# Performance work log

Measured on AMD Instinct MI355X. Metric: run time of the kernel, lower is better.

## Reference

```python
import jax, jax.numpy as jnp
import numpy as np

NUM_HEADS = 16
MODEL_DIM = 1024
DEPTH = MODEL_DIM // NUM_HEADS
B, S = 4, 1024


def setup_inputs() -> dict:
    key = jax.random.key(0)
    ks = jax.random.split(key, 12)
    sc = 1.0 / np.sqrt(MODEL_DIM)
    q = jax.random.normal(ks[0], (B, S, MODEL_DIM), jnp.float32)
    k = jax.random.normal(ks[1], (B, S, MODEL_DIM), jnp.float32)
    v = jax.random.normal(ks[2], (B, S, MODEL_DIM), jnp.float32)
    # binary padding mask, 1 = masked position (added as mask * -1e9)
    mask = (jax.random.uniform(ks[3], (B, 1, 1, S)) < 0.1).astype(jnp.float32)
    Wq = jax.random.normal(ks[4], (MODEL_DIM, MODEL_DIM), jnp.float32) * sc
    bq = jnp.zeros((MODEL_DIM,), jnp.float32)
    Wk = jax.random.normal(ks[5], (MODEL_DIM, MODEL_DIM), jnp.float32) * sc
    bk = jnp.zeros((MODEL_DIM,), jnp.float32)
    Wv = jax.random.normal(ks[6], (MODEL_DIM, MODEL_DIM), jnp.float32) * sc
    bv = jnp.zeros((MODEL_DIM,), jnp.float32)
    Wo = jax.random.normal(ks[7], (MODEL_DIM, MODEL_DIM), jnp.float32) * sc
    bo = jnp.zeros((MODEL_DIM,), jnp.float32)
    return dict(q=q, k=k, v=v, mask=mask, Wq=Wq, bq=bq, Wk=Wk, bk=bk,
                Wv=Wv, bv=bv, Wo=Wo, bo=bo)


def _split_head(x):
    b, s, _ = x.shape
    return x.reshape(b, s, NUM_HEADS, DEPTH).transpose(0, 2, 1, 3)


def reference(q, k, v, mask, Wq, bq, Wk, bk, Wv, bv, Wo, bo):
    Q = _split_head(q @ Wq + bq)   # (B,H,S,depth)
    K = _split_head(k @ Wk + bk)
    V = _split_head(v @ Wv + bv)
    # NOTE: original divides by k_dim (depth), NOT sqrt(depth) -- keep faithful
    logits = jnp.einsum('bhqd,bhkd->bhqk', Q, K) / jnp.float32(DEPTH)
    logits = logits + mask * (-1e9)
    attn = jax.nn.softmax(logits, axis=-1)         # (B,H,Sq,Sk)
    ctx = jnp.einsum('bhqk,bhkd->bhqd', attn, V)   # (B,H,S,depth)
    ctx = ctx.transpose(0, 2, 1, 3).reshape(q.shape[0], -1, MODEL_DIM)
    out = ctx @ Wo + bo
    return out, attn
```

## Files before the change

kernel.cpp:

```cpp
#include <hip/hip_runtime.h>
#include <stdint.h>
#include <stddef.h>

#define DEV __device__ __forceinline__

typedef __bf16 bf16_t;
typedef bf16_t bf16x8 __attribute__((ext_vector_type(8)));
typedef float f32x4 __attribute__((ext_vector_type(4)));
typedef unsigned short us4 __attribute__((ext_vector_type(4)));
typedef unsigned short us8 __attribute__((ext_vector_type(8)));

DEV float bf2f(unsigned short u) {
    union { unsigned int i; float f; } w; w.i = ((unsigned int)u) << 16; return w.f;
}
DEV unsigned short f2bf(float f) {
    union { unsigned int i; float f; } w; w.f = f;
    unsigned int u = w.i;
    return (unsigned short)((u + 0x7fffu + ((u >> 16) & 1u)) >> 16);
}

DEV void gl_lds16(const void* g, void* l) {
    __builtin_amdgcn_global_load_lds((const __attribute__((address_space(1))) void*)g,
                                     (__attribute__((address_space(3))) void*)l,
                                     16, 0, 0);
}

__global__ void __launch_bounds__(256)
cvt3(const float* __restrict__ s0, const float* __restrict__ s1, const float* __restrict__ s2,
     unsigned short* __restrict__ d0, unsigned short* __restrict__ d1, unsigned short* __restrict__ d2) {
    const float* src    = (blockIdx.z == 0) ? s0 : (blockIdx.z == 1) ? s1 : s2;
    unsigned short* dst = (blockIdx.z == 0) ? d0 : (blockIdx.z == 1) ? d1 : d2;
    int idx = (blockIdx.x * 256 + threadIdx.x) * 4;
    f32x4 v = *(const f32x4*)&src[idx];
    us4 o;
#pragma unroll
    for (int i = 0; i < 4; i++) o[i] = f2bf(v[i]);
    *(us4*)&dst[idx] = o;
}

__global__ void __launch_bounds__(256)
transpose_w(const float* __restrict__ W0, const float* __restrict__ W1,
            const float* __restrict__ W2, const float* __restrict__ W3,
            unsigned short* __restrict__ T0, unsigned short* __restrict__ T1,
            unsigned short* __restrict__ T2, unsigned short* __restrict__ T3) {
    const float* W    = (blockIdx.z == 0) ? W0 : (blockIdx.z == 1) ? W1 : (blockIdx.z == 2) ? W2 : W3;
    unsigned short* T = (blockIdx.z == 0) ? T0 : (blockIdx.z == 1) ? T1 : (blockIdx.z == 2) ? T2 : T3;
    __shared__ float t[32][33];
    int tx = threadIdx.x, ty = threadIdx.y;
    int k0 = blockIdx.x * 32, n0 = blockIdx.y * 32;
#pragma unroll
    for (int r = 0; r < 4; r++)
        t[ty + r * 8][tx] = W[(size_t)(k0 + ty + r * 8) * 1024 + n0 + tx];
    __syncthreads();
#pragma unroll
    for (int r = 0; r < 4; r++)
        T[(size_t)(n0 + ty + r * 8) * 1024 + k0 + tx] = f2bf(t[tx][ty + r * 8]);
}

__global__ void __launch_bounds__(256)
qkv_gemm(const unsigned short* __restrict__ Aq, const unsigned short* __restrict__ Ak,
         const unsigned short* __restrict__ Av,
         const unsigned short* __restrict__ BtQ, const unsigned short* __restrict__ BtK,
         const unsigned short* __restrict__ BtV,
         const float* __restrict__ biq, const float* __restrict__ bik,
         const float* __restrict__ biv,
         unsigned short* __restrict__ Qw, unsigned short* __restrict__ Kw,
         unsigned short* __restrict__ Vtw) {
    const int K = 1024;
    const unsigned short* A  = (blockIdx.z == 0) ? Aq  : (blockIdx.z == 1) ? Ak  : Av;
    const unsigned short* Bt = (blockIdx.z == 0) ? BtQ : (blockIdx.z == 1) ? BtK : BtV;
    const float* bias        = (blockIdx.z == 0) ? biq : (blockIdx.z == 1) ? bik : biv;
    unsigned short* Cout     = (blockIdx.z == 0) ? Qw  : (blockIdx.z == 1) ? Kw  : Vtw;
    const bool vmode = (blockIdx.z == 2);

    __shared__ __align__(16) unsigned short As[128 * 32];
    __shared__ __align__(16) unsigned short Bs[128 * 32];
    int tid = threadIdx.x, lane = tid & 63, wid = tid >> 6;
    int mBase = blockIdx.x * 128, nBase = blockIdx.y * 128;
    int wm = (wid >> 1) * 64, wn = (wid & 1) * 64;
    int c0 = lane & 15, quad = lane >> 4;

    f32x4 acc[4][4] = {};

    for (int k0 = 0; k0 < K; k0 += 32) {
        __syncthreads();
#pragma unroll
        for (int i = 0; i < 2; i++) {
            int cb = wid * 64 + 256 * i;
            int cc = cb + lane;
            int row = cc >> 2, kc = cc & 3;
            gl_lds16(A  + (size_t)(mBase + row) * K + k0 + kc * 8, &As[cb * 8]);
            gl_lds16(Bt + (size_t)(nBase + row) * K + k0 + kc * 8, &Bs[cb * 8]);
        }
        __syncthreads();
        bf16x8 af[4], bfr[4];
#pragma unroll
        for (int t = 0; t < 4; t++) {
            af[t]  = *(const bf16x8*)&As[(wm + t * 16 + c0) * 32 + quad * 8];
            bfr[t] = *(const bf16x8*)&Bs[(wn + t * 16 + c0) * 32 + quad * 8];
        }
#pragma unroll
        for (int mt = 0; mt < 4; mt++)
#pragma unroll
            for (int nt = 0; nt < 4; nt++)
                acc[mt][nt] = __builtin_amdgcn_mfma_f32_16x16x32_bf16(af[mt], bfr[nt], acc[mt][nt], 0, 0, 0);
    }

#pragma unroll
    for (int mt = 0; mt < 4; mt++) {
#pragma unroll
        for (int nt = 0; nt < 4; nt++) {
            int n = nBase + wn + nt * 16 + c0;
            float bv = bias[n];
            if (vmode) {
                int m0 = mBase + wm + mt * 16 + quad * 4;
                int b = m0 >> 10, s = m0 & 1023, h = n >> 6, d = n & 63;
                us4 pk;
#pragma unroll
                for (int r = 0; r < 4; r++) pk[r] = f2bf(acc[mt][nt][r] + bv);
                *(us4*)&Cout[((size_t)((b * 16 + h) * 64 + d)) * 1024 + s] = pk;
            } else {
#pragma unroll
                for (int r = 0; r < 4; r++) {
                    int m = mBase + wm + mt * 16 + quad * 4 + r;
                    int b = m >> 10, s = m & 1023, h = n >> 6, d = n & 63;
                    Cout[((size_t)((b * 16 + h) * 1024 + s)) * 64 + d] = f2bf(acc[mt][nt][r] + bv);
                }
            }
        }
    }
}

__global__ void __launch_bounds__(256)
out_gemm(const unsigned short* __restrict__ A,
         const unsigned short* __restrict__ Bt,
         const float* __restrict__ bias,
         float* __restrict__ Cout) {
    const int K = 1024;
    __shared__ __align__(16) unsigned short As[128 * 32];
    __shared__ __align__(16) unsigned short Bs[128 * 32];
    int tid = threadIdx.x, lane = tid & 63, wid = tid >> 6;
    int mBase = blockIdx.x * 128, nBase = blockIdx.y * 128;
    int wm = (wid >> 1) * 64, wn = (wid & 1) * 64;
    int c0 = lane & 15, quad = lane >> 4;

    f32x4 acc[4][4] = {};

    for (int k0 = 0; k0 < K; k0 += 32) {
        __syncthreads();
#pragma unroll
        for (int i = 0; i < 2; i++) {
            int cb = wid * 64 + 256 * i;
            int cc = cb + lane;
            int row = cc >> 2, kc = cc & 3;
            gl_lds16(A  + (size_t)(mBase + row) * K + k0 + kc * 8, &As[cb * 8]);
            gl_lds16(Bt + (size_t)(nBase + row) * K + k0 + kc * 8, &Bs[cb * 8]);
        }
        __syncthreads();
        bf16x8 af[4], bfr[4];
#pragma unroll
        for (int t = 0; t < 4; t++) {
            af[t]  = *(const bf16x8*)&As[(wm + t * 16 + c0) * 32 + quad * 8];
            bfr[t] = *(const bf16x8*)&Bs[(wn + t * 16 + c0) * 32 + quad * 8];
        }
#pragma unroll
        for (int mt = 0; mt < 4; mt++)
#pragma unroll
            for (int nt = 0; nt < 4; nt++)
                acc[mt][nt] = __builtin_amdgcn_mfma_f32_16x16x32_bf16(af[mt], bfr[nt], acc[mt][nt], 0, 0, 0);
    }
#pragma unroll
    for (int mt = 0; mt < 4; mt++)
#pragma unroll
        for (int nt = 0; nt < 4; nt++) {
            int n = nBase + wn + nt * 16 + c0;
            float bv = bias[n];
#pragma unroll
            for (int r = 0; r < 4; r++) {
                int m = mBase + wm + mt * 16 + quad * 4 + r;
                Cout[(size_t)m * 1024 + n] = acc[mt][nt][r] + bv;
            }
        }
}

__global__ void __launch_bounds__(256, 3)
attn_pv(const unsigned short* __restrict__ Qws,
        const unsigned short* __restrict__ Kws,
        const unsigned short* __restrict__ Vtw,
        const float* __restrict__ maskp,
        float* __restrict__ attnOut,
        unsigned short* __restrict__ ctx) {
    __shared__ __align__(16) unsigned short ldsP[17408];
    __shared__ float redbuf[4][16];

    int tid = threadIdx.x, lane = tid & 63, wid = tid >> 6;
    int c0 = lane & 15, quad = lane >> 4;
    int bh = blockIdx.y, b = bh >> 4, h = bh & 15;
    int q0 = blockIdx.x * 16;

    bf16x8 aq0, aq1;
    {
        const unsigned short* qp = Qws + ((size_t)bh * 1024 + q0 + c0) * 64 + quad * 8;
        aq0 = *(const bf16x8*)qp;
        aq1 = *(const bf16x8*)(qp + 32);
    }

    f32x4 acc[16] = {};

    for (int ch = 0; ch < 4; ch++) {
        __syncthreads();
#pragma unroll
        for (int i = 0; i < 8; i++) {
            int cb = wid * 64 + 256 * i;
            int cc = cb + lane;
            int row = cc >> 3, kc = cc & 7;
            gl_lds16(Kws + ((size_t)bh * 1024 + ch * 256 + row) * 64 + kc * 8, &ldsP[cb * 8]);
        }
        __syncthreads();
#pragma unroll
        for (int nt = 0; nt < 4; nt++) {
            int srow = wid * 64 + nt * 16 + c0;
            const unsigned short* kp = &ldsP[srow * 64 + quad * 8];
            bf16x8 b0 = *(const bf16x8*)kp;
            bf16x8 b1 = *(const bf16x8*)(kp + 32);
            int ai = ch * 4 + nt;
            acc[ai] = __builtin_amdgcn_mfma_f32_16x16x32_bf16(aq0, b0, acc[ai], 0, 0, 0);
            acc[ai] = __builtin_amdgcn_mfma_f32_16x16x32_bf16(aq1, b1, acc[ai], 0, 0, 0);
        }
    }

    float lmax[4] = {-3e38f, -3e38f, -3e38f, -3e38f};
#pragma unroll
    for (int i = 0; i < 16; i++) {
        int col = (i >> 2) * 256 + wid * 64 + (i & 3) * 16 + c0;
        float mval = maskp[b * 1024 + col] * (-1e9f);
#pragma unroll
        for (int r = 0; r < 4; r++) {
            float v = acc[i][r] * (1.0f / 64.0f) + mval;
            acc[i][r] = v;
            lmax[r] = fmaxf(lmax[r], v);
        }
    }
#pragma unroll
    for (int st = 1; st < 16; st <<= 1) {
#pragma unroll
        for (int r = 0; r < 4; r++) lmax[r] = fmaxf(lmax[r], __shfl_xor(lmax[r], st, 64));
    }
    if (c0 == 0) {
#pragma unroll
        for (int r = 0; r < 4; r++) redbuf[wid][quad * 4 + r] = lmax[r];
    }
    __syncthreads();
    float rmax[4];
#pragma unroll
    for (int r = 0; r < 4; r++) {
        int row = quad * 4 + r;
        rmax[r] = fmaxf(fmaxf(redbuf[0][row], redbuf[1][row]), fmaxf(redbuf[2][row], redbuf[3][row]));
    }
    float lsum[4] = {0.f, 0.f, 0.f, 0.f};
#pragma unroll
    for (int i = 0; i < 16; i++) {
#pragma unroll
        for (int r = 0; r < 4; r++) {
            float e = __expf(acc[i][r] - rmax[r]);
            acc[i][r] = e;
            lsum[r] += e;
        }
    }
#pragma unroll
    for (int st = 1; st < 16; st <<= 1) {
#pragma unroll
        for (int r = 0; r < 4; r++) lsum[r] += __shfl_xor(lsum[r], st, 64);
    }
    __syncthreads();
    if (c0 == 0) {
#pragma unroll
        for (int r = 0; r < 4; r++) redbuf[wid][quad * 4 + r] = lsum[r];
    }
    __syncthreads();
    float rinv[4];
#pragma unroll
    for (int r = 0; r < 4; r++) {
        int row = quad * 4 + r;
        rinv[r] = 1.0f / (redbuf[0][row] + redbuf[1][row] + redbuf[2][row] + redbuf[3][row]);
    }

    size_t gbase = ((size_t)bh * 1024 + q0) * 1024;
#pragma unroll
    for (int i = 0; i < 16; i++) {
        int kk = (i >> 2) * 64 + (i & 3) * 16 + c0;
        int col = (i >> 2) * 256 + wid * 64 + (i & 3) * 16 + c0;
        int kks = kk ^ (quad << 3);
#pragma unroll
        for (int r = 0; r < 4; r++) {
            int row = quad * 4 + r;
            float pv = acc[i][r] * rinv[r];
            attnOut[gbase + (size_t)row * 1024 + col] = pv;
            ldsP[wid * 4352 + row * 272 + kks] = f2bf(pv);
        }
    }

    const unsigned short* vbase = Vtw + ((size_t)(bh * 64 + wid * 16 + c0)) * 1024 + quad * 8;
    bf16x8 vcur[8], vnxt[8];
#pragma unroll
    for (int j = 0; j < 8; j++)
        vcur[j] = *(const bf16x8*)&vbase[(j >> 1) * 64 + (j & 1) * 32];
    __syncthreads();

    f32x4 ctx0 = {}, ctx1 = {};
#pragma unroll
    for (int ch = 0; ch < 4; ch++) {
        if (ch < 3) {
#pragma unroll
            for (int j = 0; j < 8; j++)
                vnxt[j] = *(const bf16x8*)&vbase[(ch + 1) * 256 + (j >> 1) * 64 + (j & 1) * 32];
        }
#pragma unroll
        for (int wv = 0; wv < 4; wv++) {
            int kidx0 = (ch * 64 + quad * 8) ^ ((c0 >> 2) << 3);
            int kidx1 = (ch * 64 + 32 + quad * 8) ^ ((c0 >> 2) << 3);
            bf16x8 a0 = *(const bf16x8*)&ldsP[wv * 4352 + c0 * 272 + kidx0];
            bf16x8 a1 = *(const bf16x8*)&ldsP[wv * 4352 + c0 * 272 + kidx1];
            ctx0 = __builtin_amdgcn_mfma_f32_16x16x32_bf16(a0, vcur[wv * 2 + 0], ctx0, 0, 0, 0);
            ctx1 = __builtin_amdgcn_mfma_f32_16x16x32_bf16(a1, vcur[wv * 2 + 1], ctx1, 0, 0, 0);
        }
#pragma unroll
        for (int j = 0; j < 8; j++) vcur[j] = vnxt[j];
    }
    f32x4 ctxacc = ctx0 + ctx1;

#pragma unroll
    for (int r = 0; r < 4; r++) {
        int s = q0 + quad * 4 + r;
        ctx[((size_t)(b * 1024 + s)) * 1024 + h * 64 + wid * 16 + c0] = f2bf(ctxacc[r]);
    }
}

extern "C" void kernel_launch(void* const* d_in, const int* in_sizes, int n_in,
                              void* d_out, int out_size, void* d_ws, size_t ws_size,
                              hipStream_t stream) {
    (void)in_sizes; (void)n_in; (void)out_size; (void)ws_size;
    const float* q    = (const float*)d_in[0];
    const float* k    = (const float*)d_in[1];
    const float* v    = (const float*)d_in[2];
    const float* mask = (const float*)d_in[3];
    const float* Wq   = (const float*)d_in[4];
    const float* bq   = (const float*)d_in[5];
    const float* Wk   = (const float*)d_in[6];
    const float* bk   = (const float*)d_in[7];
    const float* Wv   = (const float*)d_in[8];
    const float* bv   = (const float*)d_in[9];
    const float* Wo   = (const float*)d_in[10];
    const float* bo   = (const float*)d_in[11];

    float* outF  = (float*)d_out;
    float* attnF = outF + (size_t)4 * 1024 * 1024;

    unsigned short* wsu = (unsigned short*)d_ws;
    const size_t M1 = (size_t)1024 * 1024;
    unsigned short* WqT = wsu + 0 * M1;
    unsigned short* WkT = wsu + 1 * M1;
    unsigned short* WvT = wsu + 2 * M1;
    unsigned short* WoT = wsu + 3 * M1;
    unsigned short* tq  = wsu + 4 * M1;
    unsigned short* tk  = wsu + 8 * M1;
    unsigned short* tv  = wsu + 12 * M1;
    unsigned short* Qw  = wsu + 16 * M1;
    unsigned short* Kw  = wsu + 20 * M1;
    unsigned short* Vtw = wsu + 24 * M1;
    unsigned short* ctx = wsu + 28 * M1;

    transpose_w<<<dim3(32, 32, 4), dim3(32, 8), 0, stream>>>(Wq, Wk, Wv, Wo, WqT, WkT, WvT, WoT);

    cvt3<<<dim3(4096, 1, 3), 256, 0, stream>>>(q, k, v, tq, tk, tv);

    qkv_gemm<<<dim3(32, 8, 3), 256, 0, stream>>>(tq, tk, tv, WqT, WkT, WvT, bq, bk, bv, Qw, Kw, Vtw);

    attn_pv<<<dim3(64, 64), 256, 0, stream>>>(Qw, Kw, Vtw, mask, attnF, ctx);

    out_gemm<<<dim3(32, 8), 256, 0, stream>>>(ctx, WoT, bo, outF);
}
```

Before: 494.3 us.

## Fuse prep kernels, double GEMM K-tile with XOR-swizzled LDS layout

Merges the weight transpose and the activation fp32-to-bf16 conversion into one launch, removing a kernel launch. Both projection GEMMs now stage a 64-wide K slice per sync instead of 32, halving the number of barrier round trips. The LDS rows are XOR-swizzled to avoid bank conflicts on the wider rows. Launch bounds ask for 3 blocks per CU. The cost is twice the LDS per block and a somewhat more complex address calculation, with no double buffering, so load latency is still exposed at each barrier.

```diff
diff --git a/kernel.cpp b/kernel.cpp
--- a/kernel.cpp
+++ b/kernel.cpp
@@ -26,38 +26,44 @@
 }
 
 __global__ void __launch_bounds__(256)
-cvt3(const float* __restrict__ s0, const float* __restrict__ s1, const float* __restrict__ s2,
+prep(const float* __restrict__ W0, const float* __restrict__ W1,
+     const float* __restrict__ W2, const float* __restrict__ W3,
+     unsigned short* __restrict__ T0, unsigned short* __restrict__ T1,
+     unsigned short* __restrict__ T2, unsigned short* __restrict__ T3,
+     const float* __restrict__ s0, const float* __restrict__ s1, const float* __restrict__ s2,
      unsigned short* __restrict__ d0, unsigned short* __restrict__ d1, unsigned short* __restrict__ d2) {
-    const float* src    = (blockIdx.z == 0) ? s0 : (blockIdx.z == 1) ? s1 : s2;
-    unsigned short* dst = (blockIdx.z == 0) ? d0 : (blockIdx.z == 1) ? d1 : d2;
-    int idx = (blockIdx.x * 256 + threadIdx.x) * 4;
-    f32x4 v = *(const f32x4*)&src[idx];
-    us4 o;
-#pragma unroll
-    for (int i = 0; i < 4; i++) o[i] = f2bf(v[i]);
-    *(us4*)&dst[idx] = o;
-}
-
-__global__ void __launch_bounds__(256)
-transpose_w(const float* __restrict__ W0, const float* __restrict__ W1,
-            const float* __restrict__ W2, const float* __restrict__ W3,
-            unsigned short* __restrict__ T0, unsigned short* __restrict__ T1,
-            unsigned short* __restrict__ T2, unsigned short* __restrict__ T3) {
-    const float* W    = (blockIdx.z == 0) ? W0 : (blockIdx.z == 1) ? W1 : (blockIdx.z == 2) ? W2 : W3;
-    unsigned short* T = (blockIdx.z == 0) ? T0 : (blockIdx.z == 1) ? T1 : (blockIdx.z == 2) ? T2 : T3;
     __shared__ float t[32][33];
     int tx = threadIdx.x, ty = threadIdx.y;
-    int k0 = blockIdx.x * 32, n0 = blockIdx.y * 32;
-#pragma unroll
-    for (int r = 0; r < 4; r++)
-        t[ty + r * 8][tx] = W[(size_t)(k0 + ty + r * 8) * 1024 + n0 + tx];
-    __syncthreads();
-#pragma unroll
-    for (int r = 0; r < 4; r++)
-        T[(size_t)(n0 + ty + r * 8) * 1024 + k0 + tx] = f2bf(t[tx][ty + r * 8]);
-}
-
-__global__ void __launch_bounds__(256)
+    int z = blockIdx.z;
+    if (z < 4) {
+        const float* W    = (z == 0) ? W0 : (z == 1) ? W1 : (z == 2) ? W2 : W3;
+        unsigned short* T = (z == 0) ? T0 : (z == 1) ? T1 : (z == 2) ? T2 : T3;
+        int k0 = blockIdx.x * 32, n0 = blockIdx.y * 32;
+#pragma unroll
+        for (int r = 0; r < 4; r++)
+            t[ty + r * 8][tx] = W[(size_t)(k0 + ty + r * 8) * 1024 + n0 + tx];
+        __syncthreads();
+#pragma unroll
+        for (int r = 0; r < 4; r++)
+            T[(size_t)(n0 + ty + r * 8) * 1024 + k0 + tx] = f2bf(t[tx][ty + r * 8]);
+    } else {
+        const float* src    = (z == 4) ? s0 : (z == 5) ? s1 : s2;
+        unsigned short* dst = (z == 4) ? d0 : (z == 5) ? d1 : d2;
+        int tid = ty * 32 + tx;
+        int blk = blockIdx.y * 32 + blockIdx.x;
+#pragma unroll
+        for (int p = 0; p < 4; p++) {
+            int idx = (blk * 256 + tid) * 4 + p * 1048576;
+            f32x4 v = *(const f32x4*)&src[idx];
+            us4 o;
+#pragma unroll
+            for (int i = 0; i < 4; i++) o[i] = f2bf(v[i]);
+            *(us4*)&dst[idx] = o;
+        }
+    }
+}
+
+__global__ void __launch_bounds__(256, 3)
 qkv_gemm(const unsigned short* __restrict__ Aq, const unsigned short* __restrict__ Ak,
          const unsigned short* __restrict__ Av,
          const unsigned short* __restrict__ BtQ, const unsigned short* __restrict__ BtK,
@@ -73,8 +79,8 @@
     unsigned short* Cout     = (blockIdx.z == 0) ? Qw  : (blockIdx.z == 1) ? Kw  : Vtw;
     const bool vmode = (blockIdx.z == 2);
 
-    __shared__ __align__(16) unsigned short As[128 * 32];
-    __shared__ __align__(16) unsigned short Bs[128 * 32];
+    __shared__ __align__(16) unsigned short As[128 * 64];
+    __shared__ __align__(16) unsigned short Bs[128 * 64];
     int tid = threadIdx.x, lane = tid & 63, wid = tid >> 6;
     int mBase = blockIdx.x * 128, nBase = blockIdx.y * 128;
     int wm = (wid >> 1) * 64, wn = (wid & 1) * 64;
@@ -82,28 +88,33 @@
 
     f32x4 acc[4][4] = {};
 
-    for (int k0 = 0; k0 < K; k0 += 32) {
-        __syncthreads();
-#pragma unroll
-        for (int i = 0; i < 2; i++) {
-            int cb = wid * 64 + 256 * i;
-            int cc = cb + lane;
-            int row = cc >> 2, kc = cc & 3;
-            gl_lds16(A  + (size_t)(mBase + row) * K + k0 + kc * 8, &As[cb * 8]);
-            gl_lds16(Bt + (size_t)(nBase + row) * K + k0 + kc * 8, &Bs[cb * 8]);
-        }
-        __syncthreads();
-        bf16x8 af[4], bfr[4];
-#pragma unroll
-        for (int t = 0; t < 4; t++) {
-            af[t]  = *(const bf16x8*)&As[(wm + t * 16 + c0) * 32 + quad * 8];
-            bfr[t] = *(const bf16x8*)&Bs[(wn + t * 16 + c0) * 32 + quad * 8];
-        }
-#pragma unroll
-        for (int mt = 0; mt < 4; mt++)
-#pragma unroll
-            for (int nt = 0; nt < 4; nt++)
-                acc[mt][nt] = __builtin_amdgcn_mfma_f32_16x16x32_bf16(af[mt], bfr[nt], acc[mt][nt], 0, 0, 0);
+    for (int k0 = 0; k0 < K; k0 += 64) {
+        __syncthreads();
+#pragma unroll
+        for (int i = 0; i < 4; i++) {
+            int cc = i * 256 + tid;
+            int row = cc >> 3, kcl = cc & 7;
+            int kc = kcl ^ (row & 7);
+            gl_lds16(A  + (size_t)(mBase + row) * K + k0 + kc * 8, &As[cc * 8]);
+            gl_lds16(Bt + (size_t)(nBase + row) * K + k0 + kc * 8, &Bs[cc * 8]);
+        }
+        __syncthreads();
+#pragma unroll
+        for (int kk = 0; kk < 2; kk++) {
+            bf16x8 af[4], bfr[4];
+#pragma unroll
+            for (int t = 0; t < 4; t++) {
+                int ra = wm + t * 16 + c0;
+                int rb = wn + t * 16 + c0;
+                af[t]  = *(const bf16x8*)&As[ra * 64 + (((quad + 4 * kk) ^ (ra & 7)) << 3)];
+                bfr[t] = *(const bf16x8*)&Bs[rb * 64 + (((quad + 4 * kk) ^ (rb & 7)) << 3)];
+            }
+#pragma unroll
+            for (int mt = 0; mt < 4; mt++)
+#pragma unroll
+                for (int nt = 0; nt < 4; nt++)
+                    acc[mt][nt] = __builtin_amdgcn_mfma_f32_16x16x32_bf16(af[mt], bfr[nt], acc[mt][nt], 0, 0, 0);
+        }
     }
 
 #pragma unroll
@@ -131,14 +142,14 @@
     }
 }
 
-__global__ void __launch_bounds__(256)
+__global__ void __launch_bounds__(256, 3)
 out_gemm(const unsigned short* __restrict__ A,
          const unsigned short* __restrict__ Bt,
          const float* __restrict__ bias,
          float* __restrict__ Cout) {
     const int K = 1024;
-    __shared__ __align__(16) unsigned short As[128 * 32];
-    __shared__ __align__(16) unsigned short Bs[128 * 32];
+    __shared__ __align__(16) unsigned short As[128 * 64];
+    __shared__ __align__(16) unsigned short Bs[128 * 64];
     int tid = threadIdx.x, lane = tid & 63, wid = tid >> 6;
     int mBase = blockIdx.x * 128, nBase = blockIdx.y * 128;
     int wm = (wid >> 1) * 64, wn = (wid & 1) * 64;
@@ -146,28 +157,33 @@
 
     f32x4 acc[4][4] = {};
 
-    for (int k0 = 0; k0 < K; k0 += 32) {
-        __syncthreads();
-#pragma unroll
-        for (int i = 0; i < 2; i++) {
-            int cb = wid * 64 + 256 * i;
-            int cc = cb + lane;
-            int row = cc >> 2, kc = cc & 3;
-            gl_lds16(A  + (size_t)(mBase + row) * K + k0 + kc * 8, &As[cb * 8]);
-            gl_lds16(Bt + (size_t)(nBase + row) * K + k0 + kc * 8, &Bs[cb * 8]);
-        }
-        __syncthreads();
-        bf16x8 af[4], bfr[4];
-#pragma unroll
-        for (int t = 0; t < 4; t++) {
-            af[t]  = *(const bf16x8*)&As[(wm + t * 16 + c0) * 32 + quad * 8];
-            bfr[t] = *(const bf16x8*)&Bs[(wn + t * 16 + c0) * 32 + quad * 8];
-        }
-#pragma unroll
-        for (int mt = 0; mt < 4; mt++)
-#pragma unroll
-            for (int nt = 0; nt < 4; nt++)
-                acc[mt][nt] = __builtin_amdgcn_mfma_f32_16x16x32_bf16(af[mt], bfr[nt], acc[mt][nt], 0, 0, 0);
+    for (int k0 = 0; k0 < K; k0 += 64) {
+        __syncthreads();
+#pragma unroll
+        for (int i = 0; i < 4; i++) {
+            int cc = i * 256 + tid;
+            int row = cc >> 3, kcl = cc & 7;
+            int kc = kcl ^ (row & 7);
+            gl_lds16(A  + (size_t)(mBase + row) * K + k0 + kc * 8, &As[cc * 8]);
+            gl_lds16(Bt + (size_t)(nBase + row) * K + k0 + kc * 8, &Bs[cc * 8]);
+        }
+        __syncthreads();
+#pragma unroll
+        for (int kk = 0; kk < 2; kk++) {
+            bf16x8 af[4], bfr[4];
+#pragma unroll
+            for (int t = 0; t < 4; t++) {
+                int ra = wm + t * 16 + c0;
+                int rb = wn + t * 16 + c0;
+                af[t]  = *(const bf16x8*)&As[ra * 64 + (((quad + 4 * kk) ^ (ra & 7)) << 3)];
+                bfr[t] = *(const bf16x8*)&Bs[rb * 64 + (((quad + 4 * kk) ^ (rb & 7)) << 3)];
+            }
+#pragma unroll
+            for (int mt = 0; mt < 4; mt++)
+#pragma unroll
+                for (int nt = 0; nt < 4; nt++)
+                    acc[mt][nt] = __builtin_amdgcn_mfma_f32_16x16x32_bf16(af[mt], bfr[nt], acc[mt][nt], 0, 0, 0);
+        }
     }
 #pragma unroll
     for (int mt = 0; mt < 4; mt++)
@@ -370,9 +386,8 @@
     unsigned short* Vtw = wsu + 24 * M1;
     unsigned short* ctx = wsu + 28 * M1;
 
-    transpose_w<<<dim3(32, 32, 4), dim3(32, 8), 0, stream>>>(Wq, Wk, Wv, Wo, WqT, WkT, WvT, WoT);
-
-    cvt3<<<dim3(4096, 1, 3), 256, 0, stream>>>(q, k, v, tq, tk, tv);
+    prep<<<dim3(32, 32, 7), dim3(32, 8), 0, stream>>>(Wq, Wk, Wv, Wo, WqT, WkT, WvT, WoT,
+                                                      q, k, v, tq, tk, tv);
 
     qkv_gemm<<<dim3(32, 8, 3), 256, 0, stream>>>(tq, tk, tv, WqT, WkT, WvT, bq, bk, bv, Qw, Kw, Vtw);
 
```

Measured after the change: 475.1 us. 1.04x faster.
